# Kernel optimization log

Hardware: AMD Instinct MI355X
Metric: run time of the kernel (lower is better)

Reference implementation:

```python
import jax, jax.numpy as jnp
import numpy as np

B, C, T, Q = 4, 64, 128, 128   # batch, channels (emb_dim), frames, freq bins
K = 8                          # unfold kernel size (stride 1)
H = 128                        # SRU hidden size per direction
D_IN = C * K                   # SRU input size after unfold
L = Q - K + 1                  # unfolded sequence length
EPS = 1e-5


def setup_inputs() -> dict:
    key = jax.random.key(0)
    ks = jax.random.split(key, 6)
    s = 0.02
    return {
        "features": jax.random.normal(ks[0], (B, C, T, Q), jnp.float32),
        "ln_gamma": jnp.ones((C,), jnp.float32),
        "ln_beta": jnp.zeros((C,), jnp.float32),
        # SRU per-direction weights: W maps D_IN -> [x_tilde | f_gate | r_gate | highway], each H wide
        "w_fwd": jax.random.normal(ks[1], (D_IN, 4 * H), jnp.float32) * s,
        "b_fwd": jnp.zeros((2 * H,), jnp.float32),   # [b_f | b_r]
        "w_bwd": jax.random.normal(ks[2], (D_IN, 4 * H), jnp.float32) * s,
        "b_bwd": jnp.zeros((2 * H,), jnp.float32),
        # ConvTranspose1d weight in PyTorch layout [in_ch=2H, out_ch=C, K]
        "ct_w": jax.random.normal(ks[3], (2 * H, C, K), jnp.float32) * s,
        "ct_b": jnp.zeros((C,), jnp.float32),
    }


def _sru_dir(seq, W, b, reverse):
    """One SRU direction. seq: [N, L, D_IN] -> h: [N, L, H].
    c_t = f_t*c_{t-1} + (1-f_t)*x~_t ;  h_t = r_t*tanh(c_t) + (1-r_t)*x'_t
    (x' is the highway projection since input dim != hidden dim)."""
    U = seq @ W                                   # [N, L, 4H] -- dominant GEMM
    xt, f_pre, r_pre, xp = jnp.split(U, 4, axis=-1)
    bf, br = jnp.split(b, 2)
    f = jax.nn.sigmoid(f_pre + bf)
    r = jax.nn.sigmoid(r_pre + br)
    u = (1.0 - f) * xt
    if reverse:
        f = jnp.flip(f, 1)
        u = jnp.flip(u, 1)
    def combine(x, y):  # linear recurrence c = a*c_prev + b, y is the later element
        return (x[0] * y[0], x[1] * y[0] + y[1])
    c = jax.lax.associative_scan(combine, (f, u), axis=1)[1]
    if reverse:
        c = jnp.flip(c, 1)
    return r * jnp.tanh(c) + (1.0 - r) * xp


def reference(features, ln_gamma, ln_beta, w_fwd, b_fwd, w_bwd, b_bwd, ct_w, ct_b):
    # LayerNorm([C,1,1]): normalize over channel dim per (b,t,q)
    mu = jnp.mean(features, axis=1, keepdims=True)
    var = jnp.var(features, axis=1, keepdims=True)
    x = (features - mu) * jax.lax.rsqrt(var + EPS)
    x = x * ln_gamma[None, :, None, None] + ln_beta[None, :, None, None]

    N = B * T
    x = x.transpose(0, 2, 1, 3).reshape(N, C, Q)          # [B*T, C, Q]
    # nn.Unfold((K,1), stride 1): channel-major patch layout -> [N, C*K, L]
    u = jnp.stack([x[:, :, i:i + L] for i in range(K)], axis=2).reshape(N, C * K, L)
    seq = u.transpose(0, 2, 1)                            # [N, L, C*K]

    h = jnp.concatenate(
        [_sru_dir(seq, w_fwd, b_fwd, False), _sru_dir(seq, w_bwd, b_bwd, True)],
        axis=-1,
    )                                                      # [N, L, 2H]

    # ConvTranspose1d(2H -> C, K, stride=1) == full correlation with flipped kernel
    rhs = jnp.flip(ct_w, -1).transpose(1, 0, 2)           # [C, 2H, K]
    y = jax.lax.conv_general_dilated(
        h.transpose(0, 2, 1), rhs, (1,), [(K - 1, K - 1)],
        dimension_numbers=("NCH", "OIH", "NCH"),
    ) + ct_b[None, :, None]                               # [N, C, Q]

    y = y.reshape(B, T, C, Q).transpose(0, 2, 1, 3)       # [B, C, T, Q]
    return y + features
```

## Files before the change

### kernel.cpp

```cpp
#include <hip/hip_runtime.h>
#include <math.h>

#define BB 4
#define CC 64
#define TT 128
#define QQ 128
#define KK 8
#define HH 128
#define NN 512
#define LL 121
#define LPAD 135

typedef unsigned short ushort;
typedef __attribute__((ext_vector_type(8))) short short8;
typedef __attribute__((ext_vector_type(4))) float f32x4;
typedef __attribute__((ext_vector_type(4))) float float4v;

#define GLP(p) ((const __attribute__((address_space(1))) void*)(p))
#define LDP(p) ((__attribute__((address_space(3))) void*)(p))

__device__ __forceinline__ ushort f2bf(float x) {
  unsigned u = __float_as_uint(x);
  unsigned r = (u + 0x7FFFu + ((u >> 16) & 1u)) >> 16;
  return (ushort)r;
}

__global__ __launch_bounds__(256)
void prep_all(const float* __restrict__ f, const float* __restrict__ gamma,
              const float* __restrict__ beta, const float* __restrict__ wf,
              const float* __restrict__ wb, const float* __restrict__ ctw,
              ushort* __restrict__ xT, ushort* __restrict__ Bg,
              ushort* __restrict__ Bc2, ushort* __restrict__ zpage) {
  int bid = blockIdx.x, tid = threadIdx.x;
  if (bid < 256) {
    int p = bid * 256 + tid;
    int q = p & (QQ - 1);
    int t = (p >> 7) & (TT - 1);
    int b = p >> 14;
    const float* base = f + (size_t)b * CC * TT * QQ + (size_t)t * QQ + q;
    float v[64];
#pragma unroll
    for (int c = 0; c < 64; ++c) v[c] = base[(size_t)c * TT * QQ];
    float s = 0.f, s2 = 0.f;
#pragma unroll
    for (int c = 0; c < 64; ++c) { s += v[c]; s2 += v[c] * v[c]; }
    float mu = s * (1.f / CC);
    float var = s2 * (1.f / CC) - mu * mu;
    float rs = rsqrtf(var + 1e-5f);
    int n = b * TT + t;
    ushort* dst = xT + (size_t)n * (CC * QQ) + (size_t)q * CC;
#pragma unroll
    for (int v8 = 0; v8 < 8; ++v8) {
      short8 ov;
#pragma unroll
      for (int e = 0; e < 8; ++e) {
        int c = v8 * 8 + e;
        ov[e] = (short)f2bf((v[c] - mu) * rs * gamma[c] + beta[c]);
      }
      *(short8*)(dst + v8 * 8) = ov;
    }
  } else if (bid < 768) {
    int i = (bid - 256) * 256 + tid;
    int dir = i >> 16, r = i & 65535;
    int kidx = r >> 7, col0 = (r & 127) * 4;
    const float* w = dir ? wb : wf;
    float4v v4 = *(const float4v*)&w[(size_t)kidx * 512 + col0];
    int c = kidx >> 3, ks = kidx & 7;
    int s = c >> 5, lk = (c >> 3) & 3, e = c & 7;
    int obase = ks * 1024 + s * 512 + lk * 128 + e;
#pragma unroll
    for (int v = 0; v < 4; ++v) {
      int col = col0 + v;
      int quad = col >> 7, h = col & 127;
      int t = ((h >> 5) << 7) | (((h >> 4) & 1) << 6) | (quad << 4) | (h & 15);
      int j = dir * 512 + t;
      Bg[(size_t)(j >> 4) * 8192 + obase + (j & 15) * 8] = f2bf(v4[v]);
    }
  } else if (bid < 896) {
    int i = (bid - 768) * 256 + tid;
    int j2h = i >> 7, r = i & 127;
    int idx0 = r * 4;
    float4v v4 = *(const float4v*)&ctw[(size_t)j2h * 512 + idx0];
    int jh = j2h >> 7, rem = j2h & 127;
    int sub = rem >> 6, jo = rem & 63;
    int s = jo >> 5, lk = (jo >> 3) & 3, e = jo & 7;
    int obase = s * 2048 + lk * 512 + e;
#pragma unroll
    for (int v = 0; v < 4; ++v) {
      int idx2 = idx0 + v;
      int c = idx2 >> 3, kk = idx2 & 7;
      int win = kk * 4 + jh * 2 + sub;
      Bc2[(size_t)win * 4096 + obase + c * 8] = f2bf(v4[v]);
    }
  } else {
    if (tid < 128) ((unsigned*)zpage)[tid] = 0u;
  }
}

__global__ __launch_bounds__(256, 2)
void gemm_mfma(const ushort* __restrict__ xT, const ushort* __restrict__ Bg,
               const float* __restrict__ b_fwd, const float* __restrict__ b_bwd,
               ushort* __restrict__ hp, int n0) {
  __shared__ __align__(16) ushort Hs[144 * 64];

  int tid = threadIdx.x;
  int nl = blockIdx.y;
  int r0 = blockIdx.x * 256;
  int lane = tid & 63, w = tid >> 6;
  int lrow = lane & 15, lk = lane >> 4;
  f32x4 acc[8][4] = {};
  const ushort* xTn = xT + (size_t)(n0 + nl) * (CC * QQ);

#pragma unroll
  for (int i = 0; i < 4; ++i) {
    int p = i * 256 + tid;
    int row = p >> 3, s3 = p & 7;
    int key = ((row >> 3) ^ row) & 7;
    const ushort* g = xTn + (size_t)row * CC + (s3 ^ key) * 8;
    ushort* l = &Hs[(size_t)(i * 256 + (tid & 192)) * 8];
    __builtin_amdgcn_global_load_lds(GLP(g), LDP(l), 16, 0, 0);
  }
  if (tid < 128) {
    int p = 1024 + tid;
    int row = p >> 3, s3 = p & 7;
    int srow = row < 135 ? row : 134;
    int key = ((row >> 3) ^ row) & 7;
    const ushort* g = xTn + (size_t)srow * CC + (s3 ^ key) * 8;
    ushort* l = &Hs[(size_t)(1024 + (tid & 64)) * 8];
    __builtin_amdgcn_global_load_lds(GLP(g), LDP(l), 16, 0, 0);
  }
  __syncthreads();

  int RLb = ((lrow & 0x0C) << 3) | (lrow & 3);
  const ushort* Bw = Bg + ((size_t)(blockIdx.x * 16 + w * 4) * 8192)
                   + lk * 128 + lrow * 8;
#pragma unroll 2
  for (int ks = 0; ks < 8; ++ks) {
#pragma unroll
    for (int s = 0; s < 2; ++s) {
      short8 a[8], b[4];
#pragma unroll
      for (int nn = 0; nn < 4; ++nn)
        b[nn] = *(const short8*)&Bw[(size_t)nn * 8192 + ks * 1024 + s * 512];
#pragma unroll
      for (int m = 0; m < 8; ++m) {
        int R = RLb + m * 4 + ks;
        int key = ((R >> 3) ^ R) & 7;
        int slot = (s * 4 + lk) ^ key;
        a[m] = *(const short8*)&Hs[R * 64 + slot * 8];
      }
      __builtin_amdgcn_s_setprio(1);
#pragma unroll
      for (int m = 0; m < 8; ++m)
#pragma unroll
        for (int nn = 0; nn < 4; ++nn)
          acc[m][nn] = __builtin_amdgcn_mfma_f32_16x16x32_bf16(
              a[m], b[nn], acc[m][nn], 0, 0, 0);
      __builtin_amdgcn_s_setprio(0);
    }
  }

  int dirf = r0 >> 9;
  int hgroup = ((r0 & 511) >> 7) + (w >> 1);
  int h = hgroup * 32 + (w & 1) * 16 + lrow;
  const float* bias = dirf ? b_bwd : b_fwd;
  float bf = bias[h], br = bias[128 + h];

  float F = 1.f, U = 0.f;
  if (dirf == 0) {
#pragma unroll
    for (int m = 0; m < 8; ++m)
#pragma unroll
      for (int g = 0; g < 4; ++g) {
        int l = lk * 32 + m * 4 + g;
        float xt = acc[m][0][g], fp = acc[m][1][g];
        float fg = 1.f / (1.f + __expf(-(fp + bf)));
        float u = (1.f - fg) * xt;
        if (l > 120) { fg = 1.f; u = 0.f; }
        U = fg * U + u;
        F = fg * F;
        acc[m][0][g] = F; acc[m][1][g] = U;
      }
  } else {
#pragma unroll
    for (int m = 7; m >= 0; --m)
#pragma unroll
      for (int g = 3; g >= 0; --g) {
        int l = lk * 32 + m * 4 + g;
        float xt = acc[m][0][g], fp = acc[m][1][g];
        float fg = 1.f / (1.f + __expf(-(fp + bf)));
        float u = (1.f - fg) * xt;
        if (l > 120) { fg = 1.f; u = 0.f; }
        U = fg * U + u;
        F = fg * F;
        acc[m][0][g] = F; acc[m][1][g] = U;
      }
  }
  int e = dirf ? 3 - lk : lk;
  float lpU = 0.f;
#pragma unroll
  for (int j = 0; j < 4; ++j) {
    int jl = dirf ? 3 - j : j;
    float tF = __shfl(F, (jl << 4) + lrow);
    float tU = __shfl(U, (jl << 4) + lrow);
    if (j < e) lpU = tF * lpU + tU;
  }
  float cinit = lpU;
  ushort* hpn = hp + (size_t)nl * LPAD * 256;
  int colbase = dirf * 128 + hgroup * 32 + (w & 1) * 16;
#pragma unroll
  for (int m = 0; m < 8; ++m) {
#pragma unroll
    for (int g = 0; g < 4; ++g) {
      int l = lk * 32 + m * 4 + g;
      float c = acc[m][1][g] + acc[m][0][g] * cinit;
      float rp = acc[m][2][g];
      float rg = 1.f / (1.f + __expf(-(rp + br)));
      float e2 = __expf(2.f * c);
      float th = (e2 - 1.f) / (e2 + 1.f);
      float ho = rg * th + (1.f - rg) * acc[m][3][g];
      hpn[(size_t)(l + 7) * 256 + colbase + lrow] = f2bf(ho);
    }
  }
}

__global__ __launch_bounds__(256, 4)
void conv_mfma(const ushort* __restrict__ hp, const ushort* __restrict__ Bc2,
               const ushort* __restrict__ zpage, const float* __restrict__ ctb,
               const float* __restrict__ feat, float* __restrict__ out, int n0) {
  __shared__ __align__(16) ushort Hs[72 * 256];
  int tid = threadIdx.x;
  int qh = blockIdx.x;
  int nl = blockIdx.y;
  int lane = tid & 63, w = tid >> 6;
  int wr0 = (w >> 1) * 32, wc0 = (w & 1) * 32;
  int lrow = lane & 15, lk = lane >> 4;
  f32x4 acc[2][2] = {};
  const ushort* hpn = hp + (size_t)nl * LPAD * 256;
  const ushort* Bcw = Bc2 + lk * 512 + (wc0 + lrow) * 8;
  int qbase = qh * 64;

#pragma unroll
  for (int r = 0; r < 9; ++r) {
    int p = r * 256 + tid;
    int row = p >> 5, ck = p & 31;
    int cs = (ck & 24) | ((ck & 7) ^ (row & 7));
    int grow = qbase + row;
    const ushort* g = ((unsigned)(grow - 7) <= 120u)
        ? hpn + (size_t)grow * 256 + cs * 8
        : zpage;
    ushort* l = &Hs[(size_t)(r * 256 + (tid & 192)) * 8];
    __builtin_amdgcn_global_load_lds(GLP(g), LDP(l), 16, 0, 0);
  }
  __syncthreads();
#pragma unroll 2
  for (int t = 0; t < 32; ++t) {
    int kk = t >> 2;
    int sh = (((t >> 1) & 1) << 4) | ((t & 1) << 3);
#pragma unroll
    for (int s = 0; s < 2; ++s) {
      short8 a[2], b[2];
#pragma unroll
      for (int nn = 0; nn < 2; ++nn)
        b[nn] = *(const short8*)&Bcw[(size_t)(t * 8 + s * 4) * 512 + nn * 128];
#pragma unroll
      for (int m = 0; m < 2; ++m) {
        int row = wr0 + m * 16 + lrow + 7 - kk;
        int slot = sh | ((s * 4 + lk) ^ (row & 7));
        a[m] = *(const short8*)&Hs[row * 256 + slot * 8];
      }
#pragma unroll
      for (int m = 0; m < 2; ++m)
#pragma unroll
        for (int nn = 0; nn < 2; ++nn)
          acc[m][nn] = __builtin_amdgcn_mfma_f32_16x16x32_bf16(
              a[m], b[nn], acc[m][nn], 0, 0, 0);
    }
  }
  int n = n0 + nl;
  int b = n >> 7, tt = n & 127;
#pragma unroll
  for (int m = 0; m < 2; ++m) {
    int q0 = qbase + wr0 + m * 16 + lk * 4;
#pragma unroll
    for (int nn = 0; nn < 2; ++nn) {
      int c = wc0 + nn * 16 + lrow;
      size_t idx = (size_t)b * (CC * TT * QQ) + (size_t)c * (TT * QQ)
                 + (size_t)tt * QQ + q0;
      float4v fv = *(const float4v*)&feat[idx];
      float cb = ctb[c];
      float4v ov;
#pragma unroll
      for (int g = 0; g < 4; ++g) ov[g] = acc[m][nn][g] + cb + fv[g];
      *(float4v*)&out[idx] = ov;
    }
  }
}

extern "C" void kernel_launch(void* const* d_in, const int* in_sizes, int n_in,
                              void* d_out, int out_size, void* d_ws, size_t ws_size,
                              hipStream_t stream) {
  const float* feat  = (const float*)d_in[0];
  const float* gamma = (const float*)d_in[1];
  const float* beta  = (const float*)d_in[2];
  const float* w_fwd = (const float*)d_in[3];
  const float* b_fwd = (const float*)d_in[4];
  const float* w_bwd = (const float*)d_in[5];
  const float* b_bwd = (const float*)d_in[6];
  const float* ct_w  = (const float*)d_in[7];
  const float* ct_b  = (const float*)d_in[8];
  float* out = (float*)d_out;

  char* wsb = (char*)d_ws;
  ushort* xT  = (ushort*)wsb;
  ushort* Bg  = (ushort*)(wsb + 8389632);
  ushort* Bc2 = (ushort*)(wsb + 9438208);
  ushort* zpg = (ushort*)(wsb + 9700352);
  size_t persist = 9700864;
  size_t per_n = 69120u;
  int NC = 4;
  for (int cand = 512; cand >= 4; cand >>= 1) {
    if (persist + (size_t)cand * per_n <= ws_size) { NC = cand; break; }
  }
  ushort* hpc = (ushort*)(wsb + persist);

  prep_all<<<dim3(897), dim3(256), 0, stream>>>(feat, gamma, beta, w_fwd,
                                                w_bwd, ct_w, xT, Bg, Bc2, zpg);

  for (int n0 = 0; n0 < NN; n0 += NC) {
    gemm_mfma<<<dim3(4, NC), dim3(256), 0, stream>>>(xT, Bg, b_fwd, b_bwd,
                                                     hpc, n0);
    conv_mfma<<<dim3(2, NC), dim3(256), 0, stream>>>(hpc, Bc2, zpg, ct_b, feat,
                                                     out, n0);
  }
}
```

Measured before the change: 116.4 us.

## Split GEMM block work across sequence halves with cross-wave scan carry

Each gemm block now covers half the hidden-column groups but both halves of the sequence, with waves split by sequence half instead of column group, and the grid doubles to 8 blocks per sequence. This halves per-thread accumulators so occupancy can rise (launch bounds 3). The SRU linear-recurrence scan now needs a cross-wave carry combined through shared memory with extra syncthreads. In exchange, each block reloads the full input tile into LDS, so twice as many blocks stage the same data.

```diff
diff --git a/kernel.cpp b/kernel.cpp
--- a/kernel.cpp
+++ b/kernel.cpp
@@ -97,7 +97,7 @@
   }
 }
 
-__global__ __launch_bounds__(256, 2)
+__global__ __launch_bounds__(256, 3)
 void gemm_mfma(const ushort* __restrict__ xT, const ushort* __restrict__ Bg,
                const float* __restrict__ b_fwd, const float* __restrict__ b_bwd,
                ushort* __restrict__ hp, int n0) {
@@ -105,10 +105,12 @@
 
   int tid = threadIdx.x;
   int nl = blockIdx.y;
-  int r0 = blockIdx.x * 256;
+  int bx = blockIdx.x;
   int lane = tid & 63, w = tid >> 6;
+  int lhalf = w >> 1, jb = w & 1;
+  int wr0 = lhalf * 64;
   int lrow = lane & 15, lk = lane >> 4;
-  f32x4 acc[8][4] = {};
+  f32x4 acc[4][4] = {};
   const ushort* xTn = xT + (size_t)(n0 + nl) * (CC * QQ);
 
 #pragma unroll
@@ -131,19 +133,19 @@
   }
   __syncthreads();
 
-  int RLb = ((lrow & 0x0C) << 3) | (lrow & 3);
-  const ushort* Bw = Bg + ((size_t)(blockIdx.x * 16 + w * 4) * 8192)
+  int RLb = wr0 + (((lrow & 0x0C) << 2) | (lrow & 3));
+  const ushort* Bw = Bg + ((size_t)(bx * 8 + jb * 4) * 8192)
                    + lk * 128 + lrow * 8;
-#pragma unroll 2
+#pragma unroll 1
   for (int ks = 0; ks < 8; ++ks) {
 #pragma unroll
     for (int s = 0; s < 2; ++s) {
-      short8 a[8], b[4];
+      short8 a[4], b[4];
 #pragma unroll
       for (int nn = 0; nn < 4; ++nn)
         b[nn] = *(const short8*)&Bw[(size_t)nn * 8192 + ks * 1024 + s * 512];
 #pragma unroll
-      for (int m = 0; m < 8; ++m) {
+      for (int m = 0; m < 4; ++m) {
         int R = RLb + m * 4 + ks;
         int key = ((R >> 3) ^ R) & 7;
         int slot = (s * 4 + lk) ^ key;
@@ -151,7 +153,7 @@
       }
       __builtin_amdgcn_s_setprio(1);
 #pragma unroll
-      for (int m = 0; m < 8; ++m)
+      for (int m = 0; m < 4; ++m)
 #pragma unroll
         for (int nn = 0; nn < 4; ++nn)
           acc[m][nn] = __builtin_amdgcn_mfma_f32_16x16x32_bf16(
@@ -160,19 +162,19 @@
     }
   }
 
-  int dirf = r0 >> 9;
-  int hgroup = ((r0 & 511) >> 7) + (w >> 1);
-  int h = hgroup * 32 + (w & 1) * 16 + lrow;
+  int dirf = bx >> 2;
+  int hgroup = bx & 3;
+  int h = hgroup * 32 + jb * 16 + lrow;
   const float* bias = dirf ? b_bwd : b_fwd;
   float bf = bias[h], br = bias[128 + h];
 
   float F = 1.f, U = 0.f;
   if (dirf == 0) {
 #pragma unroll
-    for (int m = 0; m < 8; ++m)
+    for (int m = 0; m < 4; ++m)
 #pragma unroll
       for (int g = 0; g < 4; ++g) {
-        int l = lk * 32 + m * 4 + g;
+        int l = wr0 + lk * 16 + m * 4 + g;
         float xt = acc[m][0][g], fp = acc[m][1][g];
         float fg = 1.f / (1.f + __expf(-(fp + bf)));
         float u = (1.f - fg) * xt;
@@ -183,10 +185,10 @@
       }
   } else {
 #pragma unroll
-    for (int m = 7; m >= 0; --m)
+    for (int m = 3; m >= 0; --m)
 #pragma unroll
       for (int g = 3; g >= 0; --g) {
-        int l = lk * 32 + m * 4 + g;
+        int l = wr0 + lk * 16 + m * 4 + g;
         float xt = acc[m][0][g], fp = acc[m][1][g];
         float fg = 1.f / (1.f + __expf(-(fp + bf)));
         float u = (1.f - fg) * xt;
@@ -197,22 +199,30 @@
       }
   }
   int e = dirf ? 3 - lk : lk;
-  float lpU = 0.f;
+  float lpF = 1.f, lpU = 0.f;
+  float wtF = 1.f, wtU = 0.f;
 #pragma unroll
   for (int j = 0; j < 4; ++j) {
     int jl = dirf ? 3 - j : j;
     float tF = __shfl(F, (jl << 4) + lrow);
     float tU = __shfl(U, (jl << 4) + lrow);
-    if (j < e) lpU = tF * lpU + tU;
-  }
-  float cinit = lpU;
+    if (j < e) { lpU = tF * lpU + tU; lpF = lpF * tF; }
+    wtU = tF * wtU + tU; wtF = wtF * tF;
+  }
+  __syncthreads();
+  float2* wagg = (float2*)Hs;
+  if (lk == 0) wagg[(lhalf * 2 + jb) * 16 + lrow] = make_float2(wtF, wtU);
+  __syncthreads();
+  float2 Wo = wagg[((lhalf ^ 1) * 2 + jb) * 16 + lrow];
+  bool later = dirf ? (lhalf == 0) : (lhalf == 1);
+  float cinit = later ? (lpF * Wo.y + lpU) : lpU;
   ushort* hpn = hp + (size_t)nl * LPAD * 256;
-  int colbase = dirf * 128 + hgroup * 32 + (w & 1) * 16;
-#pragma unroll
-  for (int m = 0; m < 8; ++m) {
+  int colbase = dirf * 128 + hgroup * 32 + jb * 16;
+#pragma unroll
+  for (int m = 0; m < 4; ++m) {
 #pragma unroll
     for (int g = 0; g < 4; ++g) {
-      int l = lk * 32 + m * 4 + g;
+      int l = wr0 + lk * 16 + m * 4 + g;
       float c = acc[m][1][g] + acc[m][0][g] * cinit;
       float rp = acc[m][2][g];
       float rg = 1.f / (1.f + __expf(-(rp + br)));
@@ -328,7 +338,7 @@
                                                 w_bwd, ct_w, xT, Bg, Bc2, zpg);
 
   for (int n0 = 0; n0 < NN; n0 += NC) {
-    gemm_mfma<<<dim3(4, NC), dim3(256), 0, stream>>>(xT, Bg, b_fwd, b_bwd,
+    gemm_mfma<<<dim3(8, NC), dim3(256), 0, stream>>>(xT, Bg, b_fwd, b_bwd,
                                                      hpc, n0);
     conv_mfma<<<dim3(2, NC), dim3(256), 0, stream>>>(hpc, Bc2, zpg, ct_b, feat,
                                                      out, n0);
```

Measured after the change: 120.4 us. 3.4% more time.
